# Kernel tuning notes

Hardware: AMD Instinct MI355X
Metric: run time of the kernel (lower is better)

The kernel has to match this reference:

```python
import jax, jax.numpy as jnp
import numpy as np


def setup_inputs() -> dict:
    key = jax.random.key(0)
    k1, k2, k3, k4 = jax.random.split(key, 4)
    B, H_in, W_in = 512, 128, 64
    H_out, W_out, K = 256, 64, 4
    x = jax.random.normal(k1, (B, H_in, W_in), dtype=jnp.float32)
    mask = jax.random.randint(k2, (H_out, K), 0, H_in, dtype=jnp.int64)
    # stacked per-group weights (width_out, width_in*K) and biases (width_out,)
    W = jax.random.normal(k3, (H_out, W_out, W_in * K), dtype=jnp.float32) * 0.05
    b = jax.random.normal(k4, (H_out, W_out), dtype=jnp.float32) * 0.05
    return {"x": x, "mask": mask, "W": W, "b": b}


def reference(x, mask, W, b):
    # x: [B, H_in, W_in]; mask: [H_out, K]; W: [H_out, W_out, K*W_in]; b: [H_out, W_out]
    B = x.shape[0]
    H_out, K = mask.shape
    # gather rows per group: [B, H_out, K, W_in]
    gathered = x[:, mask, :]
    # flatten kernel window: [B, H_out, K*W_in]
    gathered = gathered.reshape(B, H_out, -1)
    # per-group linear: out[b,h,o] = sum_d gathered[b,h,d] * W[h,o,d] + b[h,o]
    out = jnp.einsum('bhd,hod->bho', gathered, W) + b[None, :, :]
    return out  # [B, H_out, W_out]
```

## Files before the change

### kernel.cpp

```cpp
#include <hip/hip_runtime.h>

constexpr int H_OUT = 256;
constexpr int D     = 256;

typedef __bf16 bf16x8 __attribute__((ext_vector_type(8)));
typedef float  f32x16 __attribute__((ext_vector_type(16)));

__device__ inline ushort f2bf(float f) {
    uint u = __float_as_uint(f);
    u = (u + 0x7FFFu + ((u >> 16) & 1u)) >> 16;
    return (ushort)u;
}

struct US8 { ushort s[8]; };

__device__ inline float4 pack8(float4 lo, float4 hi) {
    US8 r;
    r.s[0] = f2bf(lo.x); r.s[1] = f2bf(lo.y);
    r.s[2] = f2bf(lo.z); r.s[3] = f2bf(lo.w);
    r.s[4] = f2bf(hi.x); r.s[5] = f2bf(hi.y);
    r.s[6] = f2bf(hi.z); r.s[7] = f2bf(hi.w);
    return __builtin_bit_cast(float4, r);
}

__global__ __launch_bounds__(256, 2) void sparse_linear_mfma2(
    const float* __restrict__ x,
    const int*   __restrict__ mask,
    const float* __restrict__ W,
    const float* __restrict__ bias,
    float*       __restrict__ out)
{
    const int bx   = blockIdx.x;
    const int h    = bx & 255;
    const int half = bx >> 8;
    const int tid  = threadIdx.x;
    const int lane = tid & 63, wid = tid >> 6;
    const int wr   = (wid >> 1) * 32;
    const int wc   = (wid & 1) * 32;
    const int rowl = lane & 31, hi = lane >> 5;

    __shared__ float4 Als[2][64 * 32];

    const int rb = wc + rowl;
    const float* wp = W + ((size_t)h * 64 + rb) * D + hi * 8;
    bf16x8 bfrag[16];
    #pragma unroll
    for (int ks = 0; ks < 16; ++ks) {
        float4 lo = *(const float4*)(wp + ks * 16);
        float4 h4 = *(const float4*)(wp + ks * 16 + 4);
        bfrag[ks] = __builtin_bit_cast(bf16x8, pack8(lo, h4));
    }

    const float bv = bias[h * 64 + wc + rowl];

    const int r = tid >> 2, q = tid & 3;
    const int mrow = mask[h * 4 + q];
    const float* xrow0 = x + ((size_t)(half * 256 + r) * 128 + mrow) * 64;

    float4 xr[16];

    {
        const float4* src = (const float4*)xrow0;
        #pragma unroll
        for (int j = 0; j < 16; ++j) xr[j] = src[j];
        #pragma unroll
        for (int j = 0; j < 8; ++j) {
            const int slot = (q * 8 + j) ^ (r & 15);
            Als[0][r * 32 + slot] = pack8(xr[2 * j], xr[2 * j + 1]);
        }
    }
    __syncthreads();

    const int ra = wr + rowl;

    #pragma unroll
    for (int bt = 0; bt < 4; ++bt) {
        if (bt < 3) {
            const float4* src = (const float4*)(xrow0 + (size_t)(bt + 1) * 64 * 128 * 64);
            #pragma unroll
            for (int j = 0; j < 16; ++j) xr[j] = src[j];
        }

        f32x16 acc0 = {}, acc1 = {};
        #pragma unroll
        for (int ks = 0; ks < 16; ks += 2) {
            bf16x8 a0 = __builtin_bit_cast(bf16x8,
                Als[bt & 1][ra * 32 + ((ks * 2 + hi) ^ (ra & 15))]);
            bf16x8 a1 = __builtin_bit_cast(bf16x8,
                Als[bt & 1][ra * 32 + (((ks + 1) * 2 + hi) ^ (ra & 15))]);
            acc0 = __builtin_amdgcn_mfma_f32_32x32x16_bf16(a0, bfrag[ks],     acc0, 0, 0, 0);
            acc1 = __builtin_amdgcn_mfma_f32_32x32x16_bf16(a1, bfrag[ks + 1], acc1, 0, 0, 0);
        }

        #pragma unroll
        for (int reg = 0; reg < 16; ++reg) {
            const int rl = (reg & 3) + 8 * (reg >> 2) + 4 * hi;
            const size_t b = (size_t)half * 256 + bt * 64 + wr + rl;
            out[(b * H_OUT + h) * 64 + wc + rowl] = acc0[reg] + acc1[reg] + bv;
        }

        if (bt < 3) {
            #pragma unroll
            for (int j = 0; j < 8; ++j) {
                const int slot = (q * 8 + j) ^ (r & 15);
                Als[(bt + 1) & 1][r * 32 + slot] = pack8(xr[2 * j], xr[2 * j + 1]);
            }
        }
        __syncthreads();
    }
}

extern "C" void kernel_launch(void* const* d_in, const int* in_sizes, int n_in,
                              void* d_out, int out_size, void* d_ws, size_t ws_size,
                              hipStream_t stream) {
    const float* x    = (const float*)d_in[0];
    const int*   mask = (const int*)d_in[1];
    const float* W    = (const float*)d_in[2];
    const float* bias = (const float*)d_in[3];
    float* out = (float*)d_out;

    dim3 grid(512);
    dim3 block(256);
    sparse_linear_mfma2<<<grid, block, 0, stream>>>(x, mask, W, bias, out);
}
```

Baseline: 111.5 us.

## Stage weights in LDS with coalesced loads and single-buffer X tiles

Weights are no longer loaded straight into per-lane register fragments with strided float4 reads. The block now loads them cooperatively with coalesced float4 reads, converts them to bf16 and stores them in a swizzled LDS tile. X gathers are reorganised so each group of 16 threads reads one contiguous 256-byte row segment rather than each thread reading a whole row. The double-buffered X tile becomes a single buffer with an extra barrier, which frees registers but adds LDS reads for B fragments and more synchronisation.

```diff
diff --git a/kernel.cpp b/kernel.cpp
--- a/kernel.cpp
+++ b/kernel.cpp
@@ -12,18 +12,14 @@
     return (ushort)u;
 }
 
-struct US8 { ushort s[8]; };
-
-__device__ inline float4 pack8(float4 lo, float4 hi) {
-    US8 r;
-    r.s[0] = f2bf(lo.x); r.s[1] = f2bf(lo.y);
-    r.s[2] = f2bf(lo.z); r.s[3] = f2bf(lo.w);
-    r.s[4] = f2bf(hi.x); r.s[5] = f2bf(hi.y);
-    r.s[6] = f2bf(hi.z); r.s[7] = f2bf(hi.w);
-    return __builtin_bit_cast(float4, r);
+__device__ inline uint2 pack4(float4 v) {
+    uint2 r;
+    r.x = (uint)f2bf(v.x) | ((uint)f2bf(v.y) << 16);
+    r.y = (uint)f2bf(v.z) | ((uint)f2bf(v.w) << 16);
+    return r;
 }
 
-__global__ __launch_bounds__(256, 2) void sparse_linear_mfma2(
+__global__ __launch_bounds__(256, 2) void sparse_linear_mfma3(
     const float* __restrict__ x,
     const int*   __restrict__ mask,
     const float* __restrict__ W,
@@ -39,57 +35,70 @@
     const int wc   = (wid & 1) * 32;
     const int rowl = lane & 31, hi = lane >> 5;
 
-    __shared__ float4 Als[2][64 * 32];
+    __shared__ float4 Wls[64 * 32];
+    __shared__ float4 Xls[64 * 32];
 
-    const int rb = wc + rowl;
-    const float* wp = W + ((size_t)h * 64 + rb) * D + hi * 8;
-    bf16x8 bfrag[16];
-    #pragma unroll
-    for (int ks = 0; ks < 16; ++ks) {
-        float4 lo = *(const float4*)(wp + ks * 16);
-        float4 h4 = *(const float4*)(wp + ks * 16 + 4);
-        bfrag[ks] = __builtin_bit_cast(bf16x8, pack8(lo, h4));
+    {
+        const int wrow = tid >> 6;
+        const int c    = tid & 63;
+        const float4* wsrc = (const float4*)(W + (size_t)h * 64 * D);
+        #pragma unroll
+        for (int p = 0; p < 16; ++p) {
+            const int R = p * 4 + wrow;
+            const float4 v = wsrc[R * 64 + c];
+            const int s = c >> 1, hf = c & 1;
+            *((uint2*)&Wls[R * 32 + (s ^ (R & 15))] + hf) = pack4(v);
+        }
     }
 
-    const float bv = bias[h * 64 + wc + rowl];
-
-    const int r = tid >> 2, q = tid & 3;
-    const int mrow = mask[h * 4 + q];
-    const float* xrow0 = x + ((size_t)(half * 256 + r) * 128 + mrow) * 64;
+    const int xrr = tid >> 4;
+    const int xc  = tid & 15;
+    int mq[4];
+    #pragma unroll
+    for (int q = 0; q < 4; ++q) mq[q] = mask[h * 4 + q];
 
     float4 xr[16];
 
-    {
-        const float4* src = (const float4*)xrow0;
-        #pragma unroll
-        for (int j = 0; j < 16; ++j) xr[j] = src[j];
-        #pragma unroll
-        for (int j = 0; j < 8; ++j) {
-            const int slot = (q * 8 + j) ^ (r & 15);
-            Als[0][r * 32 + slot] = pack8(xr[2 * j], xr[2 * j + 1]);
-        }
+    #pragma unroll
+    for (int p = 0; p < 16; ++p) {
+        const int q  = p >> 2;
+        const int rr = (p & 3) * 16 + xrr;
+        xr[p] = *(const float4*)(x + ((size_t)(half * 256 + rr) * 128 + mq[q]) * 64 + xc * 4);
+    }
+    #pragma unroll
+    for (int p = 0; p < 16; ++p) {
+        const int q  = p >> 2;
+        const int rr = (p & 3) * 16 + xrr;
+        const int s  = q * 8 + (xc >> 1), hf = xc & 1;
+        *((uint2*)&Xls[rr * 32 + (s ^ (rr & 15))] + hf) = pack4(xr[p]);
     }
     __syncthreads();
 
-    const int ra = wr + rowl;
+    const int   ra = wr + rowl;
+    const int   rb = wc + rowl;
+    const float bv = bias[h * 64 + wc + rowl];
 
     #pragma unroll
     for (int bt = 0; bt < 4; ++bt) {
         if (bt < 3) {
-            const float4* src = (const float4*)(xrow0 + (size_t)(bt + 1) * 64 * 128 * 64);
             #pragma unroll
-            for (int j = 0; j < 16; ++j) xr[j] = src[j];
+            for (int p = 0; p < 16; ++p) {
+                const int q  = p >> 2;
+                const int rr = (p & 3) * 16 + xrr;
+                xr[p] = *(const float4*)(x + ((size_t)(half * 256 + (bt + 1) * 64 + rr) * 128
+                                              + mq[q]) * 64 + xc * 4);
+            }
         }
 
         f32x16 acc0 = {}, acc1 = {};
         #pragma unroll
         for (int ks = 0; ks < 16; ks += 2) {
-            bf16x8 a0 = __builtin_bit_cast(bf16x8,
-                Als[bt & 1][ra * 32 + ((ks * 2 + hi) ^ (ra & 15))]);
-            bf16x8 a1 = __builtin_bit_cast(bf16x8,
-                Als[bt & 1][ra * 32 + (((ks + 1) * 2 + hi) ^ (ra & 15))]);
-            acc0 = __builtin_amdgcn_mfma_f32_32x32x16_bf16(a0, bfrag[ks],     acc0, 0, 0, 0);
-            acc1 = __builtin_amdgcn_mfma_f32_32x32x16_bf16(a1, bfrag[ks + 1], acc1, 0, 0, 0);
+            bf16x8 a0 = __builtin_bit_cast(bf16x8, Xls[ra * 32 + ((ks * 2 + hi) ^ (ra & 15))]);
+            bf16x8 b0 = __builtin_bit_cast(bf16x8, Wls[rb * 32 + ((ks * 2 + hi) ^ (rb & 15))]);
+            bf16x8 a1 = __builtin_bit_cast(bf16x8, Xls[ra * 32 + (((ks + 1) * 2 + hi) ^ (ra & 15))]);
+            bf16x8 b1 = __builtin_bit_cast(bf16x8, Wls[rb * 32 + (((ks + 1) * 2 + hi) ^ (rb & 15))]);
+            acc0 = __builtin_amdgcn_mfma_f32_32x32x16_bf16(a0, b0, acc0, 0, 0, 0);
+            acc1 = __builtin_amdgcn_mfma_f32_32x32x16_bf16(a1, b1, acc1, 0, 0, 0);
         }
 
         #pragma unroll
@@ -100,13 +109,16 @@
         }
 
         if (bt < 3) {
+            __syncthreads();
             #pragma unroll
-            for (int j = 0; j < 8; ++j) {
-                const int slot = (q * 8 + j) ^ (r & 15);
-                Als[(bt + 1) & 1][r * 32 + slot] = pack8(xr[2 * j], xr[2 * j + 1]);
+            for (int p = 0; p < 16; ++p) {
+                const int q  = p >> 2;
+                const int rr = (p & 3) * 16 + xrr;
+                const int s  = q * 8 + (xc >> 1), hf = xc & 1;
+                *((uint2*)&Xls[rr * 32 + (s ^ (rr & 15))] + hf) = pack4(xr[p]);
             }
+            __syncthreads();
         }
-        __syncthreads();
     }
 }
 
@@ -121,5 +133,5 @@
 
     dim3 grid(512);
     dim3 block(256);
-    sparse_linear_mfma2<<<grid, block, 0, stream>>>(x, mask, W, bias, out);
+    sparse_linear_mfma3<<<grid, block, 0, stream>>>(x, mask, W, bias, out);
 }
```

After: 97.52 us. -12.5%, faster.

## Pre-convert x to bf16 and stream gathered rows directly into LDS

Applied to the files above, without the earlier changes.

A new pre-pass kernel converts all of x to bf16 in the workspace. The main kernel then gathers the masked rows with global_load_lds straight into swizzled shared memory, with the XOR swizzle folded into per-lane source addresses. This halves the bytes read by the gather and removes the register staging, the per-element conversion and the LDS store work from the main loop, so the next tile's load can overlap the MFMAs. The cost is an extra kernel launch plus a full read and write pass over x, which includes rows the mask never selects.

```diff
diff --git a/kernel.cpp b/kernel.cpp
--- a/kernel.cpp
+++ b/kernel.cpp
@@ -6,25 +6,35 @@
 typedef __bf16 bf16x8 __attribute__((ext_vector_type(8)));
 typedef float  f32x16 __attribute__((ext_vector_type(16)));
 
-__device__ inline ushort f2bf(float f) {
+__device__ __forceinline__ ushort f2bf(float f) {
     uint u = __float_as_uint(f);
     u = (u + 0x7FFFu + ((u >> 16) & 1u)) >> 16;
     return (ushort)u;
 }
-
-struct US8 { ushort s[8]; };
-
-__device__ inline float4 pack8(float4 lo, float4 hi) {
-    US8 r;
-    r.s[0] = f2bf(lo.x); r.s[1] = f2bf(lo.y);
-    r.s[2] = f2bf(lo.z); r.s[3] = f2bf(lo.w);
-    r.s[4] = f2bf(hi.x); r.s[5] = f2bf(hi.y);
-    r.s[6] = f2bf(hi.z); r.s[7] = f2bf(hi.w);
-    return __builtin_bit_cast(float4, r);
+__device__ __forceinline__ uint pack2(float a, float b) {
+    return (uint)f2bf(a) | ((uint)f2bf(b) << 16);
 }
 
-__global__ __launch_bounds__(256, 2) void sparse_linear_mfma2(
-    const float* __restrict__ x,
+__device__ __forceinline__ void gll16(const ushort* g, void* lds) {
+    __builtin_amdgcn_global_load_lds(
+        (const __attribute__((address_space(1))) uint*)g,
+        (__attribute__((address_space(3))) uint*)lds, 16, 0, 0);
+}
+
+__global__ __launch_bounds__(256) void cvt_x_bf16(
+    const float* __restrict__ x, ushort* __restrict__ xb)
+{
+    const int t = blockIdx.x * 256 + threadIdx.x;
+    const float4 a = ((const float4*)x)[2 * t];
+    const float4 b = ((const float4*)x)[2 * t + 1];
+    uint4 o;
+    o.x = pack2(a.x, a.y); o.y = pack2(a.z, a.w);
+    o.z = pack2(b.x, b.y); o.w = pack2(b.z, b.w);
+    ((uint4*)xb)[t] = o;
+}
+
+__global__ __launch_bounds__(256, 2) void sparse_linear_mfma4(
+    const ushort* __restrict__ xb,
     const int*   __restrict__ mask,
     const float* __restrict__ W,
     const float* __restrict__ bias,
@@ -39,55 +49,59 @@
     const int wc   = (wid & 1) * 32;
     const int rowl = lane & 31, hi = lane >> 5;
 
-    __shared__ float4 Als[2][64 * 32];
+    __shared__ float4 Xls[2][64 * 32];
 
-    const int rb = wc + rowl;
-    const float* wp = W + ((size_t)h * 64 + rb) * D + hi * 8;
     bf16x8 bfrag[16];
+    {
+        const float* wp = W + ((size_t)(h * 64 + wc + rowl)) * D + hi * 8;
+        #pragma unroll
+        for (int ks = 0; ks < 16; ++ks) {
+            const float4 lo = *(const float4*)(wp + ks * 16);
+            const float4 h4 = *(const float4*)(wp + ks * 16 + 4);
+            uint4 o;
+            o.x = pack2(lo.x, lo.y); o.y = pack2(lo.z, lo.w);
+            o.z = pack2(h4.x, h4.y); o.w = pack2(h4.z, h4.w);
+            bfrag[ks] = __builtin_bit_cast(bf16x8, o);
+        }
+    }
+    const float bv = bias[h * 64 + wc + rowl];
+
+    const int m0 = mask[h * 4 + 0], m1 = mask[h * 4 + 1];
+    const int m2 = mask[h * 4 + 2], m3 = mask[h * 4 + 3];
+
+    const ushort* gsrc[8];
     #pragma unroll
-    for (int ks = 0; ks < 16; ++ks) {
-        float4 lo = *(const float4*)(wp + ks * 16);
-        float4 h4 = *(const float4*)(wp + ks * 16 + 4);
-        bfrag[ks] = __builtin_bit_cast(bf16x8, pack8(lo, h4));
+    for (int i = 0; i < 8; ++i) {
+        const int rr = 16 * wid + 2 * i + hi;
+        const int c  = (lane & 31) ^ (rr & 15);
+        const int mrow = (c & 16) ? ((c & 8) ? m3 : m2) : ((c & 8) ? m1 : m0);
+        gsrc[i] = xb + ((size_t)(half * 256 + rr) * 128 + mrow) * 64 + (c & 7) * 8;
     }
 
-    const float bv = bias[h * 64 + wc + rowl];
-
-    const int r = tid >> 2, q = tid & 3;
-    const int mrow = mask[h * 4 + q];
-    const float* xrow0 = x + ((size_t)(half * 256 + r) * 128 + mrow) * 64;
-
-    float4 xr[16];
-
-    {
-        const float4* src = (const float4*)xrow0;
-        #pragma unroll
-        for (int j = 0; j < 16; ++j) xr[j] = src[j];
-        #pragma unroll
-        for (int j = 0; j < 8; ++j) {
-            const int slot = (q * 8 + j) ^ (r & 15);
-            Als[0][r * 32 + slot] = pack8(xr[2 * j], xr[2 * j + 1]);
-        }
-    }
+    #pragma unroll
+    for (int i = 0; i < 8; ++i)
+        gll16(gsrc[i], &Xls[0][(16 * wid + 2 * i) * 32]);
     __syncthreads();
 
-    const int ra = wr + rowl;
+    const int ra   = wr + rowl;
+    const int xorv = ra & 15;
 
     #pragma unroll
     for (int bt = 0; bt < 4; ++bt) {
         if (bt < 3) {
-            const float4* src = (const float4*)(xrow0 + (size_t)(bt + 1) * 64 * 128 * 64);
             #pragma unroll
-            for (int j = 0; j < 16; ++j) xr[j] = src[j];
+            for (int i = 0; i < 8; ++i) {
+                gsrc[i] += 64 * 128 * 64;
+                gll16(gsrc[i], &Xls[(bt + 1) & 1][(16 * wid + 2 * i) * 32]);
+            }
         }
 
+        const float4* xbuf = Xls[bt & 1];
         f32x16 acc0 = {}, acc1 = {};
         #pragma unroll
         for (int ks = 0; ks < 16; ks += 2) {
-            bf16x8 a0 = __builtin_bit_cast(bf16x8,
-                Als[bt & 1][ra * 32 + ((ks * 2 + hi) ^ (ra & 15))]);
-            bf16x8 a1 = __builtin_bit_cast(bf16x8,
-                Als[bt & 1][ra * 32 + (((ks + 1) * 2 + hi) ^ (ra & 15))]);
+            bf16x8 a0 = __builtin_bit_cast(bf16x8, xbuf[ra * 32 + ((ks * 2 + hi) ^ xorv)]);
+            bf16x8 a1 = __builtin_bit_cast(bf16x8, xbuf[ra * 32 + (((ks + 1) * 2 + hi) ^ xorv)]);
             acc0 = __builtin_amdgcn_mfma_f32_32x32x16_bf16(a0, bfrag[ks],     acc0, 0, 0, 0);
             acc1 = __builtin_amdgcn_mfma_f32_32x32x16_bf16(a1, bfrag[ks + 1], acc1, 0, 0, 0);
         }
@@ -99,14 +113,7 @@
             out[(b * H_OUT + h) * 64 + wc + rowl] = acc0[reg] + acc1[reg] + bv;
         }
 
-        if (bt < 3) {
-            #pragma unroll
-            for (int j = 0; j < 8; ++j) {
-                const int slot = (q * 8 + j) ^ (r & 15);
-                Als[(bt + 1) & 1][r * 32 + slot] = pack8(xr[2 * j], xr[2 * j + 1]);
-            }
-        }
-        __syncthreads();
+        if (bt < 3) __syncthreads();
     }
 }
 
@@ -117,9 +124,9 @@
     const int*   mask = (const int*)d_in[1];
     const float* W    = (const float*)d_in[2];
     const float* bias = (const float*)d_in[3];
-    float* out = (float*)d_out;
+    float*  out = (float*)d_out;
+    ushort* xb  = (ushort*)d_ws;
 
-    dim3 grid(512);
-    dim3 block(256);
-    sparse_linear_mfma2<<<grid, block, 0, stream>>>(x, mask, W, bias, out);
+    cvt_x_bf16<<<dim3(2048), dim3(256), 0, stream>>>(x, xb);
+    sparse_linear_mfma4<<<dim3(512), dim3(256), 0, stream>>>(xb, mask, W, bias, out);
 }
```

After: 101.0 us. -9.4%, faster.
